# Optimization experiments

Measured on AMD Instinct MI355X. Metric: run time of the kernel, lower is better.

Reference implementation:

```python
import jax, jax.numpy as jnp
import numpy as np

JITTER = 0.1

def se_kernel(X, X2, length_scale):
    # K[i,j] = exp(-||x_i - x2_j||^2 / length_scale^2)   (no 1/2 factor, as in source)
    Xs = X / length_scale
    X2s = X2 / length_scale
    d2 = (jnp.sum(Xs * Xs, axis=1)[:, None]
          - 2.0 * Xs @ X2s.T
          + jnp.sum(X2s * X2s, axis=1)[None, :])
    return jnp.exp(-d2)

def kron(A, B):
    # kronecker(A, B) as in source: einsum 'ab,cd->acbd' then reshape
    return jnp.einsum('ab,cd->acbd', A, B).reshape(A.shape[0] * B.shape[0], A.shape[1] * B.shape[1])

def setup_inputs() -> dict:
    key = jax.random.key(0)
    ks = jax.random.split(key, 5)
    return {
        'space_coordinates': jax.random.normal(ks[0], (150, 3), dtype=jnp.float32),
        'time_coordinates': jax.random.normal(ks[1], (40, 1), dtype=jnp.float32),
        'stData': jax.random.normal(ks[2], (150, 40), dtype=jnp.float32),
        'test_space_coordinates': jax.random.normal(ks[3], (200, 3), dtype=jnp.float32),
        'test_time_coordinates': jax.random.normal(ks[4], (30, 1), dtype=jnp.float32),
        'log_latlong_length_scale': jnp.log(jnp.asarray(1.0, dtype=jnp.float32)),
        'log_elevation_length_scale': jnp.log(jnp.asarray(1.0, dtype=jnp.float32)),
        'log_time_length_scale': jnp.log(jnp.asarray(0.25, dtype=jnp.float32)),
        'log_noise_variance': jnp.log(jnp.asarray(0.1, dtype=jnp.float32)),
        'log_signal_variance': jnp.log(jnp.asarray(1.0, dtype=jnp.float32)),
    }

def reference(space_coordinates, time_coordinates, stData,
              test_space_coordinates, test_time_coordinates,
              log_latlong_length_scale, log_elevation_length_scale,
              log_time_length_scale, log_noise_variance, log_signal_variance):
    ll = jnp.exp(log_latlong_length_scale)
    le = jnp.exp(log_elevation_length_scale)
    lt = jnp.exp(log_time_length_scale)
    Ns = space_coordinates.shape[0]
    Nt = time_coordinates.shape[0]

    # ---- update(): build sigma_inverse and alpha via Kronecker eigendecomposition ----
    spatial_K = (se_kernel(space_coordinates[:, 0:2], space_coordinates[:, 0:2], ll)
                 * se_kernel(space_coordinates[:, 2:3], space_coordinates[:, 2:3], le)
                 + JITTER * jnp.eye(Ns, dtype=space_coordinates.dtype))
    temporal_K = (se_kernel(time_coordinates, time_coordinates, lt)
                  + JITTER * jnp.eye(Nt, dtype=time_coordinates.dtype))
    ws, Vs = jnp.linalg.eigh(spatial_K)
    wt, Vt = jnp.linalg.eigh(temporal_K)
    V = kron(Vt, Vs)                                   # [N, N], N = Nt*Ns
    w = jnp.einsum('a,b->ab', wt, ws).reshape(-1)      # eigenvalues of kron kernel
    inv = 1.0 / (w + jnp.exp(log_noise_variance))
    sigma_inverse = (V * inv[None, :]) @ V.T           # V diag(inv) V^T
    alpha = sigma_inverse @ stData.T.reshape(-1, 1)    # [N, 1]

    # ---- forward ----
    test_spatial = (se_kernel(test_space_coordinates[:, 0:2], space_coordinates[:, 0:2], ll)
                    * se_kernel(test_space_coordinates[:, 2:3], space_coordinates[:, 2:3], le))
    test_temporal = se_kernel(test_time_coordinates, time_coordinates, lt)
    Kst = kron(test_temporal, test_spatial)            # [M, N], M = Mt*Ms
    yPred = Kst @ alpha                                # [M, 1]
    # fused row-wise quadratic form: diag(Kst sigma_inverse Kst^T)
    yVar = jnp.exp(log_signal_variance) - jnp.sum((Kst @ sigma_inverse) * Kst, axis=1)
    Mt = test_time_coordinates.shape[0]
    Ms = test_space_coordinates.shape[0]
    yPred = yPred.reshape(Mt, Ms).T                    # [Ms, Mt]
    yVar = yVar.reshape(Mt, Ms).T                      # [Ms, Mt]
    return (yPred, yVar)
```

## Files before the change

kernel.cpp:

```cpp
#include <hip/hip_runtime.h>
#include <math.h>

#define NS 150
#define LDW 152
#define NPACK 11848
#define NT 40
#define MS 200
#define MT 30
#define N_SWEEPS 6
#define ROUNDS (N_SWEEPS*(NT-1))
#define JITTER 0.1f
#define NTHR 512

#define WS_AW 0
#define WS_RV 1280
#define WS_QV 11520

#define OFF_MP    0
#define OFF_PR    47392
#define OFF_INVS  52256
#define OFF_DVS   52288
#define OFF_SCS   52896
#define OFF_TSCS  54704
#define OFF_GV    58704
#define OFF_WTJ   59424
#define SMEM_BYTES 59440
#define OFF_A2    0
#define OFF_VTS   13120
#define OFF_PRM   20160
#define OFF_TCS   22720

__device__ __forceinline__ int rs_off(int r) {
    int g = r >> 2, rm = r & 3;
    return LDW * r - 8 * g * (g - 1) - 4 * rm * g;
}
__device__ constexpr int rs_off_c(int r) {
    return LDW * r - 8 * (r >> 2) * ((r >> 2) - 1) - 4 * (r & 3) * (r >> 2);
}

__device__ __forceinline__ void jac_params(const float (*A)[NT+1], float4* dst,
                                           int i, int rr) {
    int i0 = i, i1 = NT - 1 - i;
    int p = (i0 == 0) ? 0 : ((i0 - 1 + rr) % (NT - 1)) + 1;
    int q = ((i1 - 1 + rr) % (NT - 1)) + 1;
    if (p > q) { int tsw = p; p = q; q = tsw; }
    float app = A[p][p], aqq = A[q][q], apq = A[p][q];
    float c, s;
    if (apq == 0.0f) { c = 1.0f; s = 0.0f; }
    else {
        float tau = (aqq - app) / (2.0f * apq);
        float tt = ((tau >= 0.0f) ? 1.0f : -1.0f) / (fabsf(tau) + sqrtf(1.0f + tau*tau));
        c = rsqrtf(1.0f + tt*tt);
        s = tt * c;
    }
    dst[i] = make_float4(c, s, __int_as_float(p), __int_as_float(q));
}

#define ST4(K0) { \
    constexpr int b0_ = rs_off_c((K0)+0) - ((K0) & ~3); \
    constexpr int b1_ = rs_off_c((K0)+1) - ((K0) & ~3); \
    constexpr int b2_ = rs_off_c((K0)+2) - ((K0) & ~3); \
    constexpr int b3_ = rs_off_c((K0)+3) - ((K0) & ~3); \
    float uk0_ = u[(K0)+0] * Mp[b0_ + (K0)+0]; \
    qa += uk0_*uk0_;  ra += uk0_ * Mp[b0_ + 150]; \
    u[(K0)+1] -= Mp[b0_ + (K0)+1] * uk0_; \
    u[(K0)+2] -= Mp[b0_ + (K0)+2] * uk0_; \
    u[(K0)+3] -= Mp[b0_ + (K0)+3] * uk0_; \
    float uk1_ = u[(K0)+1] * Mp[b1_ + (K0)+1]; \
    qa += uk1_*uk1_;  ra += uk1_ * Mp[b1_ + 150]; \
    u[(K0)+2] -= Mp[b1_ + (K0)+2] * uk1_; \
    u[(K0)+3] -= Mp[b1_ + (K0)+3] * uk1_; \
    float uk2_ = u[(K0)+2] * Mp[b2_ + (K0)+2]; \
    qa += uk2_*uk2_;  ra += uk2_ * Mp[b2_ + 150]; \
    u[(K0)+3] -= Mp[b2_ + (K0)+3] * uk2_; \
    float uk3_ = u[(K0)+3] * Mp[b3_ + (K0)+3]; \
    qa += uk3_*uk3_;  ra += uk3_ * Mp[b3_ + 150]; \
    _Pragma("unroll") \
    for (int t_ = (K0)+4; t_ < NS; t_ += 4) { \
        float4 w0_ = *(const float4*)&Mp[b0_ + t_]; \
        float4 w1_ = *(const float4*)&Mp[b1_ + t_]; \
        float4 w2_ = *(const float4*)&Mp[b2_ + t_]; \
        float4 w3_ = *(const float4*)&Mp[b3_ + t_]; \
        u[t_+0] -= w0_.x*uk0_ + w1_.x*uk1_ + w2_.x*uk2_ + w3_.x*uk3_; \
        u[t_+1] -= w0_.y*uk0_ + w1_.y*uk1_ + w2_.y*uk2_ + w3_.y*uk3_; \
        u[t_+2] -= w0_.z*uk0_ + w1_.z*uk1_ + w2_.z*uk2_ + w3_.z*uk3_; \
        u[t_+3] -= w0_.w*uk0_ + w1_.w*uk1_ + w2_.w*uk2_ + w3_.w*uk3_; \
    } \
}

#define UI(K) { \
    float d0_ = tx - scs[(K)*3+0]; \
    float d1_ = ty - scs[(K)*3+1]; \
    float d2_ = tz - scs[(K)*3+2]; \
    u[(K)] = expf(-((d0_*d0_ + d1_*d1_)*ill2 + d2_*d2_*ile2)); }
#define UI10(K) UI((K)+0) UI((K)+1) UI((K)+2) UI((K)+3) UI((K)+4) \
                UI((K)+5) UI((K)+6) UI((K)+7) UI((K)+8) UI((K)+9)

__global__ void __launch_bounds__(NTHR, 2) gp_block(
        const float* __restrict__ sc,  const float* __restrict__ tc,
        const float* __restrict__ st,  const float* __restrict__ tsc,
        const float* __restrict__ ttc,
        const float* __restrict__ lll, const float* __restrict__ lle,
        const float* __restrict__ llt, const float* __restrict__ lnv,
        float* __restrict__ ws) {
    __shared__ __align__(16) char smem[SMEM_BYTES];
    int j = blockIdx.x, tid = threadIdx.x;

    auto A2   = (float (*)[NT][NT+1])(smem + OFF_A2);
    auto Vts  = (float (*)[44])(smem + OFF_VTS);
    auto prm  = (float4 (*)[NT/2])(smem + OFF_PRM);
    float* tcs  = (float*)(smem + OFF_TCS);
    float* gv   = (float*)(smem + OFF_GV);
    float* wtjs = (float*)(smem + OFF_WTJ);
    float* scs  = (float*)(smem + OFF_SCS);
    float* tscs = (float*)(smem + OFF_TSCS);

    float ilt2 = expf(-2.0f * llt[0]);
    if (tid < NT) tcs[tid] = tc[tid];
    for (int t = tid; t < NS*3; t += NTHR) scs[t] = sc[t];
    for (int t = tid; t < MS*3; t += NTHR) tscs[t] = tsc[t];
    __syncthreads();
    for (int idx = tid; idx < NT*NT; idx += NTHR) {
        int i = idx / NT, jj = idx - i*NT;
        float dt = tcs[i] - tcs[jj];
        float v = expf(-dt*dt*ilt2);
        if (i == jj) v += JITTER;
        A2[0][i][jj] = v;
    }
    for (int idx = tid; idx < NT*44; idx += NTHR) {
        int jr = idx / 44, k = idx - jr*44;
        Vts[jr][k] = (jr == k) ? 1.0f : 0.0f;
    }
    __syncthreads();
    int wave = tid >> 6, lane = tid & 63;
    for (int rd = 0; rd < ROUNDS; ++rd) {
        int cur = rd & 1, nxt = cur ^ 1;
        float4* wp = prm[wave];
        if (lane < NT/2) jac_params(A2[cur], wp, lane, rd % (NT - 1));
        __builtin_amdgcn_wave_barrier();
        for (int t = tid; t < 600; t += NTHR) {
            if (t < 400) {
                int bi = t / 20, bj = t - bi*20;
                float4 Pi = wp[bi], Pj = wp[bj];
                int pi = __float_as_int(Pi.z), qi = __float_as_int(Pi.w);
                int pj = __float_as_int(Pj.z), qj = __float_as_int(Pj.w);
                float ci = Pi.x, si = Pi.y, cj = Pj.x, sj = Pj.y;
                float a00 = A2[cur][pi][pj], a01 = A2[cur][pi][qj];
                float a10 = A2[cur][qi][pj], a11 = A2[cur][qi][qj];
                float b00 = ci*a00 - si*a10, b01 = ci*a01 - si*a11;
                float b10 = si*a00 + ci*a10, b11 = si*a01 + ci*a11;
                A2[nxt][pi][pj] = cj*b00 - sj*b01; A2[nxt][pi][qj] = sj*b00 + cj*b01;
                A2[nxt][qi][pj] = cj*b10 - sj*b11; A2[nxt][qi][qj] = sj*b10 + cj*b11;
            } else {
                int u2 = t - 400;
                int pr = u2 / 10, ch = (u2 - pr*10) << 2;
                float4 P = wp[pr];
                int pj = __float_as_int(P.z), qj = __float_as_int(P.w);
                float c = P.x, s = P.y;
                float4 vp = *(float4*)&Vts[pj][ch];
                float4 vq = *(float4*)&Vts[qj][ch];
                float4 np, nq;
                np.x = c*vp.x - s*vq.x; nq.x = s*vp.x + c*vq.x;
                np.y = c*vp.y - s*vq.y; nq.y = s*vp.y + c*vq.y;
                np.z = c*vp.z - s*vq.z; nq.z = s*vp.z + c*vq.z;
                np.w = c*vp.w - s*vq.w; nq.w = s*vp.w + c*vq.w;
                *(float4*)&Vts[pj][ch] = np;
                *(float4*)&Vts[qj][ch] = nq;
            }
        }
        __syncthreads();
    }
    const int fin = ROUNDS & 1;
    if (tid == 0) wtjs[0] = A2[fin][j][j];
    for (int s = tid; s < NS; s += NTHR) {
        const float4* va = (const float4*)&Vts[j][0];
        const float4* sa = (const float4*)&st[s*NT];
        float acc = 0.0f;
        #pragma unroll
        for (int c4 = 0; c4 < NT/4; ++c4) {
            float4 a = va[c4], b = sa[c4];
            acc += a.x*b.x + a.y*b.y + a.z*b.z + a.w*b.w;
        }
        gv[s] = acc;
    }
    if (tid < MT) {
        float ttv = ttc[tid];
        float acc = 0.0f;
        for (int t = 0; t < NT; ++t) {
            float dt = ttv - tcs[t];
            acc += expf(-dt*dt*ilt2) * Vts[j][t];
        }
        ws[WS_AW + j*32 + tid] = acc;
    }
    __syncthreads();

    float* Mp   = (float*)(smem + OFF_MP);
    auto   Pr   = (float (*)[LDW])(smem + OFF_PR);
    float* invs = (float*)(smem + OFF_INVS);
    float* dvs  = (float*)(smem + OFF_DVS);
    float wtj = wtjs[0];
    float nv = expf(lnv[0]);
    float ill2 = expf(-2.0f * lll[0]);
    float ile2 = expf(-2.0f * lle[0]);
    for (int idx = tid; idx < NS*LDW; idx += NTHR) {
        int r = idx / LDW, c = idx - r*LDW;
        int rbase = r & ~3;
        if (c < rbase) continue;
        float v;
        if (c < NS) {
            float d0 = scs[r*3+0] - scs[c*3+0];
            float d1 = scs[r*3+1] - scs[c*3+1];
            float d2 = scs[r*3+2] - scs[c*3+2];
            v = wtj * expf(-((d0*d0 + d1*d1)*ill2 + d2*d2*ile2));
            if (c == r) v += wtj * JITTER + nv;
        } else if (c == NS) {
            v = gv[r];
        } else {
            v = 0.0f;
        }
        Mp[rs_off(r) + c - rbase] = v;
    }
    __syncthreads();
    for (int k0 = 0; k0 < NS - 1; k0 += 8) {
        int P = NS - k0; if (P > 8) P = 8;
        int W4 = (LDW - k0) >> 2;
        if (tid < W4) {
            int off[8];
            #pragma unroll
            for (int i = 0; i < 8; ++i)
                off[i] = (i < P) ? (rs_off(k0 + i) - ((i >= 4) ? 4 : 0)) : 0;
            float Bm[8][8];
            #pragma unroll
            for (int i = 0; i < 8; ++i) {
                #pragma unroll
                for (int c = 0; c < 8; ++c)
                    Bm[i][c] = (i < P && c >= i) ? Mp[off[i] + c]
                                                 : ((c == i) ? 1.0f : 0.0f);
            }
            float Lf[8][8]; float iv[8];
            #pragma unroll
            for (int k = 0; k < 8; ++k) {
                iv[k] = 1.0f / Bm[k][k];
                #pragma unroll
                for (int i = k + 1; i < 8; ++i) {
                    float l = Bm[k][i] * iv[k];
                    Lf[i][k] = l;
                    #pragma unroll
                    for (int c = i; c < 8; ++c) Bm[i][c] -= l * Bm[k][c];
                }
            }
            if (tid == 0) {
                #pragma unroll
                for (int i = 0; i < 8; ++i) invs[i] = iv[i];
            }
            int C = tid << 2;
            float4 m[8];
            #pragma unroll
            for (int i = 0; i < 8; ++i) {
                bool ok = (i < P) && (i < 4 || C >= 4);
                m[i] = ok ? *(float4*)&Mp[off[i] + C] : make_float4(0,0,0,0);
            }
            #pragma unroll
            for (int i = 1; i < 8; ++i) {
                #pragma unroll
                for (int k = 0; k < i; ++k) {
                    float l = Lf[i][k];
                    m[i].x -= l*m[k].x; m[i].y -= l*m[k].y;
                    m[i].z -= l*m[k].z; m[i].w -= l*m[k].w;
                }
            }
            #pragma unroll
            for (int i = 0; i < 8; ++i) *(float4*)&Pr[i][C] = m[i];
        }
        __syncthreads();
        for (int r = k0 + 1 + tid; r < NS; r += NTHR) {
            int rc = r - k0;
            float f[8];
            #pragma unroll
            for (int i = 0; i < 8; ++i)
                f[i] = (rc > i && i < P) ? Pr[i][rc] * invs[i] : 0.0f;
            int rbase = r & ~3;
            int ro = rs_off(r) - rbase;
            for (int C = rbase; C < LDW; C += 4) {
                int pc = C - k0;
                float4 v = *(float4*)&Mp[ro + C];
                #pragma unroll
                for (int i = 0; i < 8; ++i) {
                    float4 p = *(float4*)&Pr[i][pc];
                    v.x -= f[i]*p.x; v.y -= f[i]*p.y;
                    v.z -= f[i]*p.z; v.w -= f[i]*p.w;
                }
                *(float4*)&Mp[ro + C] = v;
            }
        }
        __syncthreads();
    }
    for (int r = tid; r < NS; r += NTHR)
        dvs[r] = rsqrtf(Mp[rs_off(r) + r - (r & ~3)]);
    __syncthreads();
    for (int idx = tid; idx < NS*LDW; idx += NTHR) {
        int r = idx / LDW, c = idx - r*LDW;
        int rbase = r & ~3;
        if (c < rbase) continue;
        int t = rs_off(r) + c - rbase;
        float dvr = dvs[r];
        if (c == r) Mp[t] = dvr;
        else if (c > r) Mp[t] *= dvr;
    }
    __syncthreads();
    if (tid < MS) {
        float tx = tscs[tid*3+0], ty = tscs[tid*3+1], tz = tscs[tid*3+2];
        float u[152];
        UI10(0)  UI10(10) UI10(20) UI10(30) UI10(40)
        UI10(50) UI10(60) UI10(70) UI10(80) UI10(90)
        UI10(100) UI10(110) UI10(120) UI10(130) UI10(140)
        u[150] = 0.0f; u[151] = 0.0f;
        float qa = 0.0f, ra = 0.0f;
        ST4(0)   ST4(4)   ST4(8)   ST4(12)  ST4(16)  ST4(20)  ST4(24)
        ST4(28)  ST4(32)  ST4(36)  ST4(40)  ST4(44)  ST4(48)  ST4(52)
        ST4(56)  ST4(60)  ST4(64)  ST4(68)  ST4(72)  ST4(76)  ST4(80)
        ST4(84)  ST4(88)  ST4(92)  ST4(96)  ST4(100) ST4(104) ST4(108)
        ST4(112) ST4(116) ST4(120) ST4(124) ST4(128) ST4(132) ST4(136)
        ST4(140) ST4(144)
        {
            constexpr int b8_ = rs_off_c(148) - 148;
            constexpr int b9_ = rs_off_c(149) - 148;
            float uk8_ = u[148] * Mp[b8_ + 148];
            qa += uk8_*uk8_;  ra += uk8_ * Mp[b8_ + 150];
            u[149] -= Mp[b8_ + 149] * uk8_;
            float uk9_ = u[149] * Mp[b9_ + 149];
            qa += uk9_*uk9_;  ra += uk9_ * Mp[b9_ + 150];
        }
        ws[WS_RV + j*256 + tid] = ra;
        ws[WS_QV + j*256 + tid] = qa;
    }
}

__global__ void __launch_bounds__(256) gp_reduce(
        const float* __restrict__ ws, const float* __restrict__ lsv,
        float* __restrict__ out) {
    int idx = blockIdx.x * 256 + threadIdx.x;
    if (idx >= MS*MT) return;
    int is = idx / MT, it = idx - is*MT;
    float p = 0.0f, q = 0.0f;
    #pragma unroll
    for (int jj = 0; jj < NT; ++jj) {
        float a = ws[WS_AW + jj*32 + it];
        p += a * ws[WS_RV + jj*256 + is];
        q += a * a * ws[WS_QV + jj*256 + is];
    }
    out[idx] = p;
    out[MS*MT + idx] = expf(lsv[0]) - q;
}

extern "C" void kernel_launch(void* const* d_in, const int* in_sizes, int n_in,
                              void* d_out, int out_size, void* d_ws, size_t ws_size,
                              hipStream_t stream) {
    const float* sc  = (const float*)d_in[0];
    const float* tc  = (const float*)d_in[1];
    const float* st  = (const float*)d_in[2];
    const float* tsc = (const float*)d_in[3];
    const float* ttc = (const float*)d_in[4];
    const float* lll = (const float*)d_in[5];
    const float* lle = (const float*)d_in[6];
    const float* llt = (const float*)d_in[7];
    const float* lnv = (const float*)d_in[8];
    const float* lsv = (const float*)d_in[9];
    float* out = (float*)d_out;
    float* ws  = (float*)d_ws;

    hipLaunchKernelGGL(gp_block, dim3(NT), dim3(NTHR), 0, stream,
                       sc, tc, st, tsc, ttc, lll, lle, llt, lnv, ws);
    hipLaunchKernelGGL(gp_reduce, dim3((MS*MT + 255)/256), dim3(256), 0, stream,
                       ws, lsv, out);
}
```

Before: 414.4 us.

## Broadcast Jacobi rotation params via wave shuffles and widen block to 704 threads

Each wave now computes the 20 Jacobi rotation parameters in registers and distributes them with __shfl instead of writing them to a per-wave shared-memory table and issuing a wave barrier. The block grows from 512 to 704 threads so that the A-update (400 threads, waves 0-6) and the V-update (200 threads, waves 7-10) each run in a single pass with no strided loop. This removes LDS traffic and the wave barrier from each of the 234 rounds. In exchange every wave repeats the parameter computation, and the larger block may reduce occupancy under launch_bounds(NTHR,2) or raise register pressure.

```diff
diff --git a/kernel.cpp b/kernel.cpp
--- a/kernel.cpp
+++ b/kernel.cpp
@@ -3,14 +3,13 @@
 
 #define NS 150
 #define LDW 152
-#define NPACK 11848
 #define NT 40
 #define MS 200
 #define MT 30
 #define N_SWEEPS 6
 #define ROUNDS (N_SWEEPS*(NT-1))
 #define JITTER 0.1f
-#define NTHR 512
+#define NTHR 704
 
 #define WS_AW 0
 #define WS_RV 1280
@@ -27,8 +26,7 @@
 #define SMEM_BYTES 59440
 #define OFF_A2    0
 #define OFF_VTS   13120
-#define OFF_PRM   20160
-#define OFF_TCS   22720
+#define OFF_TCS   20160
 
 __device__ __forceinline__ int rs_off(int r) {
     int g = r >> 2, rm = r & 3;
@@ -36,24 +34,6 @@
 }
 __device__ constexpr int rs_off_c(int r) {
     return LDW * r - 8 * (r >> 2) * ((r >> 2) - 1) - 4 * (r & 3) * (r >> 2);
-}
-
-__device__ __forceinline__ void jac_params(const float (*A)[NT+1], float4* dst,
-                                           int i, int rr) {
-    int i0 = i, i1 = NT - 1 - i;
-    int p = (i0 == 0) ? 0 : ((i0 - 1 + rr) % (NT - 1)) + 1;
-    int q = ((i1 - 1 + rr) % (NT - 1)) + 1;
-    if (p > q) { int tsw = p; p = q; q = tsw; }
-    float app = A[p][p], aqq = A[q][q], apq = A[p][q];
-    float c, s;
-    if (apq == 0.0f) { c = 1.0f; s = 0.0f; }
-    else {
-        float tau = (aqq - app) / (2.0f * apq);
-        float tt = ((tau >= 0.0f) ? 1.0f : -1.0f) / (fabsf(tau) + sqrtf(1.0f + tau*tau));
-        c = rsqrtf(1.0f + tt*tt);
-        s = tt * c;
-    }
-    dst[i] = make_float4(c, s, __int_as_float(p), __int_as_float(q));
 }
 
 #define ST4(K0) { \
@@ -108,7 +88,6 @@
 
     auto A2   = (float (*)[NT][NT+1])(smem + OFF_A2);
     auto Vts  = (float (*)[44])(smem + OFF_VTS);
-    auto prm  = (float4 (*)[NT/2])(smem + OFF_PRM);
     float* tcs  = (float*)(smem + OFF_TCS);
     float* gv   = (float*)(smem + OFF_GV);
     float* wtjs = (float*)(smem + OFF_WTJ);
@@ -132,31 +111,52 @@
         Vts[jr][k] = (jr == k) ? 1.0f : 0.0f;
     }
     __syncthreads();
-    int wave = tid >> 6, lane = tid & 63;
+
+    int lane = tid & 63;
+    int wv = tid >> 6;
     for (int rd = 0; rd < ROUNDS; ++rd) {
         int cur = rd & 1, nxt = cur ^ 1;
-        float4* wp = prm[wave];
-        if (lane < NT/2) jac_params(A2[cur], wp, lane, rd % (NT - 1));
-        __builtin_amdgcn_wave_barrier();
-        for (int t = tid; t < 600; t += NTHR) {
-            if (t < 400) {
-                int bi = t / 20, bj = t - bi*20;
-                float4 Pi = wp[bi], Pj = wp[bj];
-                int pi = __float_as_int(Pi.z), qi = __float_as_int(Pi.w);
-                int pj = __float_as_int(Pj.z), qj = __float_as_int(Pj.w);
-                float ci = Pi.x, si = Pi.y, cj = Pj.x, sj = Pj.y;
+        int rr = rd % (NT - 1);
+        float pcv, psv; int ppv, pqv;
+        {
+            int i0 = (lane < NT/2) ? lane : 0;
+            int p = (i0 == 0) ? 0 : ((i0 - 1 + rr) % (NT - 1)) + 1;
+            int i1 = NT - 1 - i0;
+            int q = ((i1 - 1 + rr) % (NT - 1)) + 1;
+            if (p > q) { int tsw = p; p = q; q = tsw; }
+            float app = A2[cur][p][p], aqq = A2[cur][q][q], apq = A2[cur][p][q];
+            float c, s;
+            if (apq == 0.0f) { c = 1.0f; s = 0.0f; }
+            else {
+                float tau = (aqq - app) / (2.0f * apq);
+                float tt = ((tau >= 0.0f) ? 1.0f : -1.0f)
+                           / (fabsf(tau) + sqrtf(1.0f + tau*tau));
+                c = rsqrtf(1.0f + tt*tt);
+                s = tt * c;
+            }
+            pcv = c; psv = s; ppv = p; pqv = q;
+        }
+        if (wv <= 6) {
+            int ta = (tid < 400) ? tid : 0;
+            int bi = ta / 20, bj = ta - bi*20;
+            float ci = __shfl(pcv, bi), si = __shfl(psv, bi);
+            int   pi = __shfl(ppv, bi), qi = __shfl(pqv, bi);
+            float cj = __shfl(pcv, bj), sj = __shfl(psv, bj);
+            int   pj = __shfl(ppv, bj), qj = __shfl(pqv, bj);
+            if (tid < 400) {
                 float a00 = A2[cur][pi][pj], a01 = A2[cur][pi][qj];
                 float a10 = A2[cur][qi][pj], a11 = A2[cur][qi][qj];
                 float b00 = ci*a00 - si*a10, b01 = ci*a01 - si*a11;
                 float b10 = si*a00 + ci*a10, b11 = si*a01 + ci*a11;
                 A2[nxt][pi][pj] = cj*b00 - sj*b01; A2[nxt][pi][qj] = sj*b00 + cj*b01;
                 A2[nxt][qi][pj] = cj*b10 - sj*b11; A2[nxt][qi][qj] = sj*b10 + cj*b11;
-            } else {
-                int u2 = t - 400;
-                int pr = u2 / 10, ch = (u2 - pr*10) << 2;
-                float4 P = wp[pr];
-                int pj = __float_as_int(P.z), qj = __float_as_int(P.w);
-                float c = P.x, s = P.y;
+            }
+        } else {
+            int tvv = (tid >= 448 && tid < 648) ? (tid - 448) : 0;
+            int pr = tvv / 10, ch = (tvv - pr*10) << 2;
+            float c = __shfl(pcv, pr), s = __shfl(psv, pr);
+            int  pj = __shfl(ppv, pr), qj = __shfl(pqv, pr);
+            if (tid < 648) {
                 float4 vp = *(float4*)&Vts[pj][ch];
                 float4 vq = *(float4*)&Vts[qj][ch];
                 float4 np, nq;
```

New measurement: 620.9 us. +49.8%, slower.
